# Kernel optimization log

Measured on AMD Instinct MI355X. Metric: run time of the kernel, lower is better.

## Reference

```python
import jax, jax.numpy as jnp
import numpy as np

B, S, H, NH = 4, 2048, 1024, 16
HD = H // NH
EPS = 1e-12

def setup_inputs() -> dict:
    key = jax.random.key(0)
    ks = jax.random.split(key, 8)
    sc = 1.0 / np.sqrt(H)
    return {
        "input_tensor": jax.random.normal(ks[0], (B, S, H), jnp.float32),
        "attention_mask": jnp.zeros((B, 1, 1, S), jnp.float32),
        "Wq": jax.random.normal(ks[1], (H, H), jnp.float32) * sc,
        "bq": jnp.zeros((H,), jnp.float32),
        "Wk": jax.random.normal(ks[2], (H, H), jnp.float32) * sc,
        "bk": jnp.zeros((H,), jnp.float32),
        "Wv": jax.random.normal(ks[3], (H, H), jnp.float32) * sc,
        "bv": jnp.zeros((H,), jnp.float32),
        "Wo": jax.random.normal(ks[4], (H, H), jnp.float32) * sc,
        "bo": jnp.zeros((H,), jnp.float32),
        "ln_w": jnp.ones((H,), jnp.float32),
        "ln_b": jnpp_zeros if False else jnp.zeros((H,), jnp.float32),
    }

def reference(input_tensor, attention_mask, Wq, bq, Wk, bk, Wv, bv, Wo, bo, ln_w, ln_b):
    x = input_tensor  # [B,S,H]
    # QKV projections (torch Linear: x @ W.T + b), split heads -> [B,S,NH,HD]
    q = (x @ Wq.T + bq).reshape(B, S, NH, HD)
    k = (x @ Wk.T + bk).reshape(B, S, NH, HD)
    v = (x @ Wv.T + bv).reshape(B, S, NH, HD)
    # scores [B,NH,S,S]
    scores = jnp.einsum('bqhd,bkhd->bhqk', q, k) / jnp.sqrt(jnp.float32(HD))
    scores = scores + attention_mask  # broadcast [B,1,1,S]
    probs = jax.nn.softmax(scores, axis=-1)  # dropout is identity in eval
    ctx = jnp.einsum('bhqk,bkhd->bqhd', probs, v).reshape(B, S, H)
    # output dense + residual + LayerNorm (TF-style eps inside sqrt)
    h = ctx @ Wo.T + bo + x
    u = h.mean(-1, keepdims=True)
    s = jnp.mean((h - u) ** 2, axis=-1, keepdims=True)
    return ln_w * (h - u) / jnp.sqrt(s + EPS) + ln_b
```

## Files before the change

kernel.cpp:

```cpp
#include <hip/hip_runtime.h>

typedef __bf16 bf16;
typedef __bf16 bf16x8 __attribute__((ext_vector_type(8)));
typedef __bf16 bf16x4 __attribute__((ext_vector_type(4)));
typedef float floatx4 __attribute__((ext_vector_type(4)));
typedef int   intx4  __attribute__((ext_vector_type(4)));
typedef int   intx2  __attribute__((ext_vector_type(2)));

#define MFMA16(a,b,c) __builtin_amdgcn_mfma_f32_16x16x32_bf16((a),(b),(c),0,0,0)

constexpr int Bc  = 4;
constexpr int Sc  = 2048;
constexpr int Hc  = 1024;
constexpr int NHc = 16;
constexpr int HDc = 64;
constexpr int Mc  = Bc * Sc;
constexpr int KIT = Hc / 32;
constexpr float L2E = 1.44269504088896f;

union U64  { bf16x4 h; intx2 i; };

__device__ __forceinline__ void ld16(const bf16* g, bf16* l) {
    __builtin_amdgcn_global_load_lds(
        (const __attribute__((address_space(1))) void*)g,
        (__attribute__((address_space(3))) void*)l, 16, 0, 0);
}

__global__ void detect_k(const unsigned short* __restrict__ x, int* __restrict__ flag)
{
    if (threadIdx.x == 0 && blockIdx.x == 0) {
        float mx = 0.f;
        for (int i = 0; i < 256; ++i) {
            unsigned int bits = ((unsigned int)x[i]) << 16;
            float v = __uint_as_float(bits);
            if (!isfinite(v)) { mx = 1e30f; break; }
            mx = fmaxf(mx, fabsf(v));
        }
        *flag = (mx > 1e6f) ? 1 : 0;
    }
}

__global__ __launch_bounds__(256)
void conv_all_k(const void* __restrict__ x,
                const void* __restrict__ Wq, const void* __restrict__ Wk,
                const void* __restrict__ Wv, const void* __restrict__ Wo,
                const void* __restrict__ mask,
                const void* __restrict__ bq, const void* __restrict__ bk,
                const void* __restrict__ bv, const void* __restrict__ bo,
                const void* __restrict__ lnw, const void* __restrict__ lnb,
                bf16* __restrict__ xb, bf16* __restrict__ wdst,
                float* maskf, float* bqf, float* bkf, float* bvf,
                float* bof, float* lnwf, float* lnbf,
                const int* __restrict__ flag)
{
    const int g = blockIdx.x * 256 + threadIdx.x;
    const int fl = *flag;
    if (g < 1048576) {
        if (fl) {
            const float* s = (const float*)x + (size_t)g * 8;
            union { intx4 v; bf16 e[8]; } o;
#pragma unroll
            for (int j = 0; j < 8; ++j) o.e[j] = (bf16)s[j];
            *(intx4*)(xb + (size_t)g * 8) = o.v;
        } else {
            *(intx4*)(xb + (size_t)g * 8) = *((const intx4*)x + g);
        }
    } else if (g < 1048576 + 524288) {
        const int gw = g - 1048576;
        const int wsel = gw >> 17, go = gw & 131071;
        const void* s = (wsel == 0) ? Wq : (wsel == 1) ? Wk : (wsel == 2) ? Wv : Wo;
        if (fl) {
            const float* sp = (const float*)s + (size_t)go * 8;
            union { intx4 v; bf16 e[8]; } o;
#pragma unroll
            for (int j = 0; j < 8; ++j) o.e[j] = (bf16)sp[j];
            *(intx4*)(wdst + (size_t)gw * 8) = o.v;
        } else {
            *(intx4*)(wdst + (size_t)gw * 8) = *((const intx4*)s + go);
        }
    } else {
        const int gs = g - 1048576 - 524288;
        if (gs >= 1792) return;
        const void* src; float* dst; int off; float scl = 1.0f;
        if (gs < 1024) { src = mask; dst = maskf; off = gs * 8; scl = L2E; }
        else {
            const int a = (gs - 1024) >> 7;
            off = ((gs - 1024) & 127) * 8;
            switch (a) {
                case 0: src = bq;  dst = bqf;  break;
                case 1: src = bk;  dst = bkf;  break;
                case 2: src = bv;  dst = bvf;  break;
                case 3: src = bo;  dst = bof;  break;
                case 4: src = lnw; dst = lnwf; break;
                default: src = lnb; dst = lnbf; break;
            }
        }
        if (fl) {
            const float* s = (const float*)src + off;
#pragma unroll
            for (int j = 0; j < 8; ++j) dst[off + j] = s[j] * scl;
        } else {
            union { intx4 v; bf16 e[8]; } u;
            u.v = *(const intx4*)((const bf16*)src + off);
#pragma unroll
            for (int j = 0; j < 8; ++j) dst[off + j] = (float)u.e[j] * scl;
        }
    }
}

template<int SWAP>
__device__ __forceinline__
void gemm_core(const bf16* __restrict__ A, const bf16* __restrict__ W,
               int m0, int n0, int t, bf16* As, bf16* Bs, floatx4 (&acc)[4][4])
{
    const int l  = t & 63, w = t >> 6;
    const int wr = w >> 1, wc = w & 1;
    const int lq = l >> 4, ln = l & 15;
    const int srow = t >> 2;
    const int scol = (t & 3) * 8;

    const bf16* a0 = A + (size_t)(m0 + srow) * Hc + scol;
    const bf16* b0 = W + (size_t)(n0 + srow) * Hc + scol;
    bf16* lA0 = As + srow * 32 + scol;
    bf16* lA1 = lA0 + 64 * 32;
    bf16* lB0 = Bs + srow * 32 + scol;
    bf16* lB1 = lB0 + 64 * 32;

    for (int kb = 0; kb < KIT; ++kb) {
        const int off = kb * 32;
        ld16(a0 + off,           lA0);
        ld16(a0 + 64 * Hc + off, lA1);
        ld16(b0 + off,           lB0);
        ld16(b0 + 64 * Hc + off, lB1);
        __syncthreads();

        bf16x8 af[4], bw[4];
#pragma unroll
        for (int i = 0; i < 4; ++i)
            af[i] = *(const bf16x8*)&As[(wr * 64 + i * 16 + ln) * 32 + lq * 8];
#pragma unroll
        for (int j = 0; j < 4; ++j)
            bw[j] = *(const bf16x8*)&Bs[(wc * 64 + j * 16 + ln) * 32 + lq * 8];
#pragma unroll
        for (int i = 0; i < 4; ++i)
#pragma unroll
            for (int j = 0; j < 4; ++j)
                acc[i][j] = SWAP ? MFMA16(bw[j], af[i], acc[i][j])
                                 : MFMA16(af[i], bw[j], acc[i][j]);
        __syncthreads();
    }
}

__global__ __launch_bounds__(256)
void qkv_gemm(const bf16* __restrict__ x,
              const bf16* __restrict__ Wq, const float* __restrict__ bq,
              const bf16* __restrict__ Wk, const float* __restrict__ bk,
              const bf16* __restrict__ Wv, const float* __restrict__ bv,
              bf16* __restrict__ qo, bf16* __restrict__ ko, bf16* __restrict__ vto)
{
    __shared__ __align__(16) bf16 smem[8704];
    const int z = blockIdx.z;
    const bf16*  W    = (z == 0) ? Wq : (z == 1) ? Wk : Wv;
    const float* bias = (z == 0) ? bq : (z == 1) ? bk : bv;

    const int m0 = blockIdx.y * 128, n0 = blockIdx.x * 128;
    const int t  = threadIdx.x;
    const int l  = t & 63, w = t >> 6;
    const int wr = w >> 1, wc = w & 1;
    const int lq = l >> 4, ln = l & 15;

    if (z < 2) {
        floatx4 acc[4][4] = {};
        gemm_core<1>(x, W, m0, n0, t, smem, smem + 4096, acc);
        bf16* out = (z == 0) ? qo : ko;
        const float sc = (z == 0) ? 0.125f * L2E : 1.0f;
#pragma unroll
        for (int j = 0; j < 4; ++j) {
            const int feat = n0 + wc * 64 + j * 16 + lq * 4;
            const floatx4 bb = *(const floatx4*)&bias[feat];
            const int hh = feat >> 6, dd = feat & 63;
#pragma unroll
            for (int i = 0; i < 4; ++i) {
                const int xrow = m0 + wr * 64 + i * 16 + ln;
                const int bi = xrow >> 11, si = xrow & (Sc - 1);
                U64 pk;
#pragma unroll
                for (int r = 0; r < 4; ++r) pk.h[r] = (bf16)((acc[i][j][r] + bb[r]) * sc);
                *(intx2*)&out[(((size_t)bi * NHc + hh) * Sc + si) * HDc + dd] = pk.i;
            }
        }
    } else {
        floatx4 acc[4][4] = {};
        gemm_core<0>(x, W, m0, n0, t, smem, smem + 4096, acc);
        bf16* Ct = smem;
        const int bi = m0 >> 11, s0 = m0 & (Sc - 1);
        for (int h2 = 0; h2 < 2; ++h2) {
            __syncthreads();
            if (wc == h2) {
#pragma unroll
                for (int j = 0; j < 4; ++j) {
                    const int c = j * 16 + ln;
                    const float bb = bias[n0 + h2 * 64 + c];
#pragma unroll
                    for (int i = 0; i < 4; ++i) {
                        U64 pk;
#pragma unroll
                        for (int r = 0; r < 4; ++r) pk.h[r] = (bf16)(acc[i][j][r] + bb);
                        *(intx2*)&Ct[c * 136 + wr * 64 + i * 16 + lq * 4] = pk.i;
                    }
                }
            }
            __syncthreads();
#pragma unroll
            for (int u = 0; u < 4; ++u) {
                const int id = t + 256 * u;
                const int c = id >> 4, rg = id & 15;
                const int hh = (n0 >> 6) + h2;
                intx4 val = *(const intx4*)&Ct[c * 136 + rg * 8];
                *(intx4*)&vto[(((size_t)bi * NHc + hh) * HDc + c) * Sc + s0 + rg * 8] = val;
            }
        }
    }
}

__global__ __launch_bounds__(256)
void oproj_gemm(const bf16* __restrict__ ctx, const bf16* __restrict__ Wo,
                const float* __restrict__ bo, const bf16* __restrict__ xb,
                bf16* __restrict__ hout)
{
    __shared__ __align__(16) bf16 smem[8192];
    const int m0 = blockIdx.y * 128, n0 = blockIdx.x * 128;
    const int t  = threadIdx.x;
    floatx4 acc[4][4] = {};
    gemm_core<1>(ctx, Wo, m0, n0, t, smem, smem + 4096, acc);

    const int l  = t & 63, w = t >> 6;
    const int wr = w >> 1, wc = w & 1;
    const int lq = l >> 4, ln = l & 15;
#pragma unroll
    for (int j = 0; j < 4; ++j) {
        const int col = n0 + wc * 64 + j * 16 + lq * 4;
        const floatx4 bb = *(const floatx4*)&bo[col];
#pragma unroll
        for (int i = 0; i < 4; ++i) {
            const int row = m0 + wr * 64 + i * 16 + ln;
            U64 rx;
            rx.i = *(const intx2*)&xb[(size_t)row * Hc + col];
            U64 pk;
#pragma unroll
            for (int r = 0; r < 4; ++r)
                pk.h[r] = (bf16)(acc[i][j][r] + bb[r] + (float)rx.h[r]);
            *(intx2*)&hout[(size_t)row * Hc + col] = pk.i;
        }
    }
}

__global__ __launch_bounds__(256, 2)
void attention(const bf16* __restrict__ q, const bf16* __restrict__ k,
               const bf16* __restrict__ vt, const float* __restrict__ maskf,
               bf16* __restrict__ ctx)
{
    __shared__ __align__(16) bf16 KV[2][2][64][64];

    const int raw = blockIdx.x;
    const int xcd = raw & 7, jj = raw >> 3;
    const int bh  = xcd * 8 + (jj >> 3);
    const int qt  = jj & 7;
    const int b = bh >> 4, h = bh & 15;
    const int t = threadIdx.x, w = t >> 6, l = t & 63;
    const int lq = l >> 4, ln = l & 15;
    const int q0 = qt * 256 + w * 64;

    const bf16* kg = k  + (size_t)bh * Sc * HDc;
    const bf16* vg = vt + (size_t)bh * HDc * Sc;
    const float* mbase = maskf + b * Sc;

    const int rr  = l >> 3;
    const int gsw = ((l & 7) ^ rr) << 3;
    const int r0  = w * 16 + rr, r1 = r0 + 8;
    const int dco = (l & 7) << 3;

    bf16x8 qf[4][2];
#pragma unroll
    for (int qb = 0; qb < 4; ++qb)
#pragma unroll
        for (int kh = 0; kh < 2; ++kh)
            qf[qb][kh] = *(const bf16x8*)(q + ((size_t)bh * Sc + q0 + qb * 16 + ln) * HDc
                                            + kh * 32 + lq * 8);

    floatx4 o[4][4] = {};
    float dacc[4] = {0.f, 0.f, 0.f, 0.f};

    auto stage = [&](int buf, int kt) {
        bf16* Kd = &KV[buf][0][0][0];
        bf16* Vd = &KV[buf][1][0][0];
        ld16(kg + (size_t)(kt * 64 + r0) * HDc + gsw, Kd + r0 * 64 + dco);
        ld16(kg + (size_t)(kt * 64 + r1) * HDc + gsw, Kd + r1 * 64 + dco);
        ld16(vg + (size_t)r0 * Sc + kt * 64 + gsw,    Vd + r0 * 64 + dco);
        ld16(vg + (size_t)r1 * Sc + kt * 64 + gsw,    Vd + r1 * 64 + dco);
    };

    stage(0, 0);
    int cur = 0;

    for (int kt = 0; kt < Sc / 64; ++kt) {
        __syncthreads();
        if (kt + 1 < Sc / 64) stage(cur ^ 1, kt + 1);

        const bf16* Kb = &KV[cur][0][0][0];
        const bf16* Vb = &KV[cur][1][0][0];

        floatx4 mvl[4];
#pragma unroll
        for (int cb = 0; cb < 4; ++cb)
            mvl[cb] = *(const floatx4*)(mbase + kt * 64 + cb * 16 + lq * 4);

        bf16x8 kf[4][2], vf[4][2];
        const int sw = ln & 7;
#pragma unroll
        for (int cb = 0; cb < 4; ++cb) {
            const int row = (cb * 16 + ln) * 64;
#pragma unroll
            for (int kh = 0; kh < 2; ++kh) {
                const int cc = ((kh * 4 + lq) ^ sw) << 3;
                kf[cb][kh] = *(const bf16x8*)&Kb[row + cc];
                vf[cb][kh] = *(const bf16x8*)&Vb[row + cc];
            }
        }

        __builtin_amdgcn_s_setprio(1);
#pragma unroll
        for (int qb = 0; qb < 4; ++qb) {
            floatx4 s[4];
#pragma unroll
            for (int cb = 0; cb < 4; ++cb) {
                s[cb] = mvl[cb];
                s[cb] = MFMA16(kf[cb][0], qf[qb][0], s[cb]);
                s[cb] = MFMA16(kf[cb][1], qf[qb][1], s[cb]);
            }
            unsigned int D[4][2];
            float ds = 0.f;
#pragma unroll
            for (int cb = 0; cb < 4; ++cb)
#pragma unroll
                for (int i = 0; i < 2; ++i) {
                    const float e0 = __builtin_amdgcn_exp2f(s[cb][2 * i]);
                    const float e1 = __builtin_amdgcn_exp2f(s[cb][2 * i + 1]);
                    ds += e0 + e1;
                    union { unsigned int u; bf16 e[2]; } pk2;
                    pk2.e[0] = (bf16)e0; pk2.e[1] = (bf16)e1;
                    D[cb][i] = pk2.u;
                }
            dacc[qb] += ds;

            unsigned int F0[4], F1[4];
            {
                unsigned int A, B;
                A = D[0][0]; B = D[1][0];
                asm("v_permlane32_swap_b32 %0, %1" : "+v"(A), "+v"(B));
                asm("v_permlane16_swap_b32 %0, %1" : "+v"(A), "+v"(B));
                F0[0] = A; F0[2] = B;
                A = D[0][1]; B = D[1][1];
                asm("v_permlane32_swap_b32 %0, %1" : "+v"(A), "+v"(B));
                asm("v_permlane16_swap_b32 %0, %1" : "+v"(A), "+v"(B));
                F0[1] = A; F0[3] = B;
                A = D[2][0]; B = D[3][0];
                asm("v_permlane32_swap_b32 %0, %1" : "+v"(A), "+v"(B));
                asm("v_permlane16_swap_b32 %0, %1" : "+v"(A), "+v"(B));
                F1[0] = A; F1[2] = B;
                A = D[2][1]; B = D[3][1];
                asm("v_permlane32_swap_b32 %0, %1" : "+v"(A), "+v"(B));
                asm("v_permlane16_swap_b32 %0, %1" : "+v"(A), "+v"(B));
                F1[1] = A; F1[3] = B;
            }
            union { unsigned int u[4]; bf16x8 v; } P0, P1;
#pragma unroll
            for (int d = 0; d < 4; ++d) { P0.u[d] = F0[d]; P1.u[d] = F1[d]; }
            const bf16x8 pf0 = P0.v, pf1 = P1.v;

#pragma unroll
            for (int db = 0; db < 4; ++db) {
                o[qb][db] = MFMA16(vf[db][0], pf0, o[qb][db]);
                o[qb][db] = MFMA16(vf[db][1], pf1, o[qb][db]);
            }
        }
        __builtin_amdgcn_s_setprio(0);
        cur ^= 1;
    }

#pragma unroll
    for (int qb = 0; qb < 4; ++qb) {
        float dsum = dacc[qb];
        dsum += __shfl_xor(dsum, 16, 64);
        dsum += __shfl_xor(dsum, 32, 64);
        const float li = 1.f / dsum;
        const int qg = q0 + qb * 16 + ln;
#pragma unroll
        for (int db = 0; db < 4; ++db) {
            U64 pk;
#pragma unroll
            for (int r = 0; r < 4; ++r) pk.h[r] = (bf16)(o[qb][db][r] * li);
            *(intx2*)&ctx[((size_t)b * Sc + qg) * Hc + h * HDc + db * 16 + lq * 4] = pk.i;
        }
    }
}

__global__ __launch_bounds__(256)
void layernorm_k(const bf16* __restrict__ hbuf, const float* __restrict__ lw,
                 const float* __restrict__ lb, void* __restrict__ outp,
                 const int* __restrict__ flag)
{
    const int row = blockIdx.x;
    const int t = threadIdx.x;
    const bf16* hp = hbuf + (size_t)row * Hc;

    union { intx2 i2; bf16 e[4]; } pk;
    pk.i2 = *(const intx2*)(hp + t * 4);
    float v[4], sum = 0.f, sq = 0.f;
#pragma unroll
    for (int i = 0; i < 4; ++i) {
        v[i] = (float)pk.e[i];
        sum += v[i];
        sq  += v[i] * v[i];
    }
#pragma unroll
    for (int off = 1; off < 64; off <<= 1) {
        sum += __shfl_xor(sum, off, 64);
        sq  += __shfl_xor(sq,  off, 64);
    }
    __shared__ float ssum[4], ssq[4];
    const int w = t >> 6;
    if ((t & 63) == 0) { ssum[w] = sum; ssq[w] = sq; }
    __syncthreads();
    sum = ssum[0] + ssum[1] + ssum[2] + ssum[3];
    sq  = ssq[0]  + ssq[1]  + ssq[2]  + ssq[3];

    const float mean = sum * (1.f / (float)Hc);
    const float var  = sq * (1.f / (float)Hc) - mean * mean;
    const float rstd = rsqrtf(var + 1e-12f);

    float ov[4];
#pragma unroll
    for (int i = 0; i < 4; ++i) {
        const int c = t * 4 + i;
        ov[i] = lw[c] * (v[i] - mean) * rstd + lb[c];
    }
    if (*flag) {
        float* of = (float*)outp + (size_t)row * Hc + t * 4;
#pragma unroll
        for (int i = 0; i < 4; ++i) of[i] = ov[i];
    } else {
        union { intx2 i2; bf16 e[4]; } po;
#pragma unroll
        for (int i = 0; i < 4; ++i) po.e[i] = (bf16)ov[i];
        *(intx2*)((bf16*)outp + (size_t)row * Hc + t * 4) = po.i2;
    }
}

extern "C" void kernel_launch(void* const* d_in, const int* in_sizes, int n_in,
                              void* d_out, int out_size, void* d_ws, size_t ws_size,
                              hipStream_t stream)
{
    const void* x    = d_in[0];
    const void* mask = d_in[1];
    const void* Wq   = d_in[2];
    const void* bq   = d_in[3];
    const void* Wk   = d_in[4];
    const void* bk   = d_in[5];
    const void* Wv   = d_in[6];
    const void* bv   = d_in[7];
    const void* Wo   = d_in[8];
    const void* bo   = d_in[9];
    const void* lnw  = d_in[10];
    const void* lnb  = d_in[11];

    char* ws = (char*)d_ws;
    const size_t MB = 1024 * 1024;
    int*   flag  = (int*)ws;
    float* maskf = (float*)(ws + 4096);
    float* bqf   = (float*)(ws + 64 * 1024);
    float* bkf   = bqf + Hc;
    float* bvf   = bkf + Hc;
    float* bof   = bvf + Hc;
    float* lnwf  = bof + Hc;
    float* lnbf  = lnwf + Hc;
    bf16* xb  = (bf16*)(ws + 1 * MB);
    bf16* wqb = (bf16*)(ws + 17 * MB);
    bf16* wkb = (bf16*)(ws + 19 * MB);
    bf16* wvb = (bf16*)(ws + 21 * MB);
    bf16* wob = (bf16*)(ws + 23 * MB);
    bf16* qb  = (bf16*)(ws + 25 * MB);
    bf16* kb  = (bf16*)(ws + 41 * MB);
    bf16* vtb = (bf16*)(ws + 57 * MB);
    bf16* cb  = (bf16*)(ws + 73 * MB);
    bf16* hb  = qb;

    detect_k<<<1, 64, 0, stream>>>((const unsigned short*)x, flag);

    conv_all_k<<<6153, 256, 0, stream>>>(x, Wq, Wk, Wv, Wo, mask,
                                         bq, bk, bv, bo, lnw, lnb,
                                         xb, wqb, maskf, bqf, bkf, bvf,
                                         bof, lnwf, lnbf, flag);

    dim3 gqkv(Hc / 128, Mc / 128, 3);
    qkv_gemm<<<gqkv, 256, 0, stream>>>(xb, wqb, bqf, wkb, bkf, wvb, bvf, qb, kb, vtb);
    attention<<<dim3(Bc * NHc * (Sc / 256)), 256, 0, stream>>>(qb, kb, vtb, maskf, cb);
    oproj_gemm<<<dim3(Hc / 128, Mc / 128), 256, 0, stream>>>(cb, wob, bof, xb, hb);
    layernorm_k<<<dim3(Mc), 256, 0, stream>>>(hb, lnwf, lnbf, d_out, flag);
}
```

Measured before the change: 342.6 us.

## Double-buffer GEMM LDS loads, remap tiles per XCD, shrink attention tiles for occupancy

```diff
diff --git a/kernel.cpp b/kernel.cpp
--- a/kernel.cpp
+++ b/kernel.cpp
@@ -121,34 +121,52 @@
 
     const bf16* a0 = A + (size_t)(m0 + srow) * Hc + scol;
     const bf16* b0 = W + (size_t)(n0 + srow) * Hc + scol;
-    bf16* lA0 = As + srow * 32 + scol;
-    bf16* lA1 = lA0 + 64 * 32;
-    bf16* lB0 = Bs + srow * 32 + scol;
-    bf16* lB1 = lB0 + 64 * 32;
-
+    const int dst = srow * 32 + scol;
+
+    auto stage = [&](int buf, int kb) {
+        const int off = kb * 32;
+        bf16* dA = As + buf * 4096;
+        bf16* dB = Bs + buf * 4096;
+        ld16(a0 + off,           dA + dst);
+        ld16(a0 + 64 * Hc + off, dA + 64 * 32 + dst);
+        ld16(b0 + off,           dB + dst);
+        ld16(b0 + 64 * Hc + off, dB + 64 * 32 + dst);
+    };
+
+    stage(0, 0);
+    int cur = 0;
     for (int kb = 0; kb < KIT; ++kb) {
-        const int off = kb * 32;
-        ld16(a0 + off,           lA0);
-        ld16(a0 + 64 * Hc + off, lA1);
-        ld16(b0 + off,           lB0);
-        ld16(b0 + 64 * Hc + off, lB1);
         __syncthreads();
-
+        if (kb + 1 < KIT) stage(cur ^ 1, kb + 1);
+
+        const bf16* Ab = As + cur * 4096;
+        const bf16* Bb = Bs + cur * 4096;
         bf16x8 af[4], bw[4];
 #pragma unroll
         for (int i = 0; i < 4; ++i)
-            af[i] = *(const bf16x8*)&As[(wr * 64 + i * 16 + ln) * 32 + lq * 8];
+            af[i] = *(const bf16x8*)&Ab[(wr * 64 + i * 16 + ln) * 32 + lq * 8];
 #pragma unroll
         for (int j = 0; j < 4; ++j)
-            bw[j] = *(const bf16x8*)&Bs[(wc * 64 + j * 16 + ln) * 32 + lq * 8];
+            bw[j] = *(const bf16x8*)&Bb[(wc * 64 + j * 16 + ln) * 32 + lq * 8];
+
+        __builtin_amdgcn_s_setprio(1);
 #pragma unroll
         for (int i = 0; i < 4; ++i)
 #pragma unroll
             for (int j = 0; j < 4; ++j)
                 acc[i][j] = SWAP ? MFMA16(bw[j], af[i], acc[i][j])
                                  : MFMA16(af[i], bw[j], acc[i][j]);
-        __syncthreads();
-    }
+        __builtin_amdgcn_s_setprio(0);
+        cur ^= 1;
+    }
+}
+
+__device__ __forceinline__ void xcd_remap(int bx, int by, int& m0, int& n0)
+{
+    const int flat = by * 8 + bx;
+    const int sw   = (flat & 7) * 64 + (flat >> 3);
+    m0 = (sw >> 3) * 128;
+    n0 = (sw & 7) * 128;
 }
 
 __global__ __launch_bounds__(256)
@@ -158,12 +176,13 @@
               const bf16* __restrict__ Wv, const float* __restrict__ bv,
               bf16* __restrict__ qo, bf16* __restrict__ ko, bf16* __restrict__ vto)
 {
-    __shared__ __align__(16) bf16 smem[8704];
+    __shared__ __align__(16) bf16 smem[16384];
     const int z = blockIdx.z;
     const bf16*  W    = (z == 0) ? Wq : (z == 1) ? Wk : Wv;
     const float* bias = (z == 0) ? bq : (z == 1) ? bk : bv;
 
-    const int m0 = blockIdx.y * 128, n0 = blockIdx.x * 128;
+    int m0, n0;
+    xcd_remap(blockIdx.x, blockIdx.y, m0, n0);
     const int t  = threadIdx.x;
     const int l  = t & 63, w = t >> 6;
     const int wr = w >> 1, wc = w & 1;
@@ -171,7 +190,7 @@
 
     if (z < 2) {
         floatx4 acc[4][4] = {};
-        gemm_core<1>(x, W, m0, n0, t, smem, smem + 4096, acc);
+        gemm_core<1>(x, W, m0, n0, t, smem, smem + 8192, acc);
         bf16* out = (z == 0) ? qo : ko;
         const float sc = (z == 0) ? 0.125f * L2E : 1.0f;
 #pragma unroll
@@ -191,7 +210,7 @@
         }
     } else {
         floatx4 acc[4][4] = {};
-        gemm_core<0>(x, W, m0, n0, t, smem, smem + 4096, acc);
+        gemm_core<0>(x, W, m0, n0, t, smem, smem + 8192, acc);
         bf16* Ct = smem;
         const int bi = m0 >> 11, s0 = m0 & (Sc - 1);
         for (int h2 = 0; h2 < 2; ++h2) {
@@ -228,11 +247,12 @@
                 const float* __restrict__ bo, const bf16* __restrict__ xb,
                 bf16* __restrict__ hout)
 {
-    __shared__ __align__(16) bf16 smem[8192];
-    const int m0 = blockIdx.y * 128, n0 = blockIdx.x * 128;
+    __shared__ __align__(16) bf16 smem[16384];
+    int m0, n0;
+    xcd_remap(blockIdx.x, blockIdx.y, m0, n0);
     const int t  = threadIdx.x;
     floatx4 acc[4][4] = {};
-    gemm_core<1>(ctx, Wo, m0, n0, t, smem, smem + 4096, acc);
+    gemm_core<1>(ctx, Wo, m0, n0, t, smem, smem + 8192, acc);
 
     const int l  = t & 63, w = t >> 6;
     const int wr = w >> 1, wc = w & 1;
@@ -255,7 +275,7 @@
     }
 }
 
-__global__ __launch_bounds__(256, 2)
+__global__ __launch_bounds__(256, 4)
 void attention(const bf16* __restrict__ q, const bf16* __restrict__ k,
                const bf16* __restrict__ vt, const float* __restrict__ maskf,
                bf16* __restrict__ ctx)
@@ -264,12 +284,12 @@
 
     const int raw = blockIdx.x;
     const int xcd = raw & 7, jj = raw >> 3;
-    const int bh  = xcd * 8 + (jj >> 3);
-    const int qt  = jj & 7;
+    const int bh  = xcd * 8 + (jj >> 4);
+    const int qt  = jj & 15;
     const int b = bh >> 4, h = bh & 15;
     const int t = threadIdx.x, w = t >> 6, l = t & 63;
     const int lq = l >> 4, ln = l & 15;
-    const int q0 = qt * 256 + w * 64;
+    const int q0 = qt * 128 + w * 32;
 
     const bf16* kg = k  + (size_t)bh * Sc * HDc;
     const bf16* vg = vt + (size_t)bh * HDc * Sc;
@@ -280,16 +300,16 @@
     const int r0  = w * 16 + rr, r1 = r0 + 8;
     const int dco = (l & 7) << 3;
 
-    bf16x8 qf[4][2];
-#pragma unroll
-    for (int qb = 0; qb < 4; ++qb)
+    bf16x8 qf[2][2];
+#pragma unroll
+    for (int qb = 0; qb < 2; ++qb)
 #pragma unroll
         for (int kh = 0; kh < 2; ++kh)
             qf[qb][kh] = *(const bf16x8*)(q + ((size_t)bh * Sc + q0 + qb * 16 + ln) * HDc
                                             + kh * 32 + lq * 8);
 
-    floatx4 o[4][4] = {};
-    float dacc[4] = {0.f, 0.f, 0.f, 0.f};
+    floatx4 o[2][4] = {};
+    float dacc[2] = {0.f, 0.f};
 
     auto stage = [&](int buf, int kt) {
         bf16* Kd = &KV[buf][0][0][0];
@@ -302,6 +322,7 @@
 
     stage(0, 0);
     int cur = 0;
+    const int sw = ln & 7;
 
     for (int kt = 0; kt < Sc / 64; ++kt) {
         __syncthreads();
@@ -310,42 +331,42 @@
         const bf16* Kb = &KV[cur][0][0][0];
         const bf16* Vb = &KV[cur][1][0][0];
 
-        floatx4 mvl[4];
-#pragma unroll
-        for (int cb = 0; cb < 4; ++cb)
-            mvl[cb] = *(const floatx4*)(mbase + kt * 64 + cb * 16 + lq * 4);
-
-        bf16x8 kf[4][2], vf[4][2];
-        const int sw = ln & 7;
+        floatx4 s[2][4];
 #pragma unroll
         for (int cb = 0; cb < 4; ++cb) {
-            const int row = (cb * 16 + ln) * 64;
-#pragma unroll
-            for (int kh = 0; kh < 2; ++kh) {
+            const floatx4 mv = *(const floatx4*)(mbase + kt * 64 + cb * 16 + lq * 4);
+            s[0][cb] = mv;
+            s[1][cb] = mv;
+        }
+
+#pragma unroll
+        for (int kh = 0; kh < 2; ++kh) {
+            bf16x8 kf[4];
+#pragma unroll
+            for (int cb = 0; cb < 4; ++cb) {
                 const int cc = ((kh * 4 + lq) ^ sw) << 3;
-                kf[cb][kh] = *(const bf16x8*)&Kb[row + cc];
-                vf[cb][kh] = *(const bf16x8*)&Vb[row + cc];
-            }
-        }
-
-        __builtin_amdgcn_s_setprio(1);
-#pragma unroll
-        for (int qb = 0; qb < 4; ++qb) {
-            floatx4 s[4];
-#pragma unroll
-            for (int cb = 0; cb < 4; ++cb) {
-                s[cb] = mvl[cb];
-                s[cb] = MFMA16(kf[cb][0], qf[qb][0], s[cb]);
-                s[cb] = MFMA16(kf[cb][1], qf[qb][1], s[cb]);
-            }
+                kf[cb] = *(const bf16x8*)&Kb[(cb * 16 + ln) * 64 + cc];
+            }
+            __builtin_amdgcn_s_setprio(1);
+#pragma unroll
+            for (int qb = 0; qb < 2; ++qb)
+#pragma unroll
+                for (int cb = 0; cb < 4; ++cb)
+                    s[qb][cb] = MFMA16(kf[cb], qf[qb][kh], s[qb][cb]);
+            __builtin_amdgcn_s_setprio(0);
+        }
+
+        bf16x8 pf[2][2];
+#pragma unroll
+        for (int qb = 0; qb < 2; ++qb) {
             unsigned int D[4][2];
             float ds = 0.f;
 #pragma unroll
             for (int cb = 0; cb < 4; ++cb)
 #pragma unroll
                 for (int i = 0; i < 2; ++i) {
-                    const float e0 = __builtin_amdgcn_exp2f(s[cb][2 * i]);
-                    const float e1 = __builtin_amdgcn_exp2f(s[cb][2 * i + 1]);
+                    const float e0 = __builtin_amdgcn_exp2f(s[qb][cb][2 * i]);
+                    const float e1 = __builtin_amdgcn_exp2f(s[qb][cb][2 * i + 1]);
                     ds += e0 + e1;
                     union { unsigned int u; bf16 e[2]; } pk2;
                     pk2.e[0] = (bf16)e0; pk2.e[1] = (bf16)e1;
@@ -376,20 +397,31 @@
             union { unsigned int u[4]; bf16x8 v; } P0, P1;
 #pragma unroll
             for (int d = 0; d < 4; ++d) { P0.u[d] = F0[d]; P1.u[d] = F1[d]; }
-            const bf16x8 pf0 = P0.v, pf1 = P1.v;
-
+            pf[qb][0] = P0.v;
+            pf[qb][1] = P1.v;
+        }
+
+#pragma unroll
+        for (int kh = 0; kh < 2; ++kh) {
+            bf16x8 vf[4];
 #pragma unroll
             for (int db = 0; db < 4; ++db) {
-                o[qb][db] = MFMA16(vf[db][0], pf0, o[qb][db]);
-                o[qb][db] = MFMA16(vf[db][1], pf1, o[qb][db]);
-            }
-        }
-        __builtin_amdgcn_s_setprio(0);
+                const int cc = ((kh * 4 + lq) ^ sw) << 3;
+                vf[db] = *(const bf16x8*)&Vb[(db * 16 + ln) * 64 + cc];
+            }
+            __builtin_amdgcn_s_setprio(1);
+#pragma unroll
+            for (int qb = 0; qb < 2; ++qb)
+#pragma unroll
+                for (int db = 0; db < 4; ++db)
+                    o[qb][db] = MFMA16(vf[db], pf[qb][kh], o[qb][db]);
+            __builtin_amdgcn_s_setprio(0);
+        }
         cur ^= 1;
     }
 
 #pragma unroll
-    for (int qb = 0; qb < 4; ++qb) {
+    for (int qb = 0; qb < 2; ++qb) {
         float dsum = dacc[qb];
         dsum += __shfl_xor(dsum, 16, 64);
         dsum += __shfl_xor(dsum, 32, 64);
@@ -504,7 +536,7 @@
 
     dim3 gqkv(Hc / 128, Mc / 128, 3);
     qkv_gemm<<<gqkv, 256, 0, stream>>>(xb, wqb, bqf, wkb, bkf, wvb, bvf, qb, kb, vtb);
-    attention<<<dim3(Bc * NHc * (Sc / 256)), 256, 0, stream>>>(qb, kb, vtb, maskf, cb);
+    attention<<<dim3(Bc * NHc * (Sc / 128)), 256, 0, stream>>>(qb, kb, vtb, maskf, cb);
     oproj_gemm<<<dim3(Hc / 128, Mc / 128), 256, 0, stream>>>(cb, wob, bof, xb, hb);
     layernorm_k<<<dim3(Mc), 256, 0, stream>>>(hb, lnwf, lnbf, d_out, flag);
 }
```

Result: no change. 342.0 us (-0.2%).
